# Optimization experiments

Hardware: AMD Instinct MI355X
Metric: run time of the kernel (lower is better)

## Reference

```python
import jax, jax.numpy as jnp
import numpy as np

HEADS = 16  # init kwarg 'heads'

def setup_inputs() -> dict:
    key = jax.random.key(0)
    k1, k2, k3 = jax.random.split(key, 3)
    B, S, D = 2, 2048, 1024
    x = jax.random.normal(k1, (B, S, D), dtype=jnp.float32)
    # nn.Linear(dim, 3*dim, bias=False): y = x @ W^T; store as [D, 3D] already transposed.
    w_qkv = jax.random.normal(k2, (D, 3 * D), dtype=jnp.float32) * 0.02
    w_out = jax.random.normal(k3, (D, D), dtype=jnp.float32) * 0.02
    return {"x": x, "w_qkv": w_qkv, "w_out": w_out}

def reference(x, w_qkv, w_out):
    B, S, D = x.shape
    H = HEADS
    hd = D // H
    scale = 1.0 / jnp.sqrt(jnp.asarray(hd, dtype=x.dtype))
    qkv = x @ w_qkv                      # [B, S, 3D]
    q, k, v = jnp.split(qkv, 3, axis=-1)
    def to_heads(t):
        return t.reshape(B, S, H, hd).transpose(0, 2, 1, 3)  # [B, H, S, hd]
    q, k, v = to_heads(q), to_heads(k), to_heads(v)
    scores = jnp.einsum('bhqd,bhkd->bhqk', q, k) * scale      # [B, H, S, S]
    # causal mask: query i attends to keys j <= i
    causal = jnp.tril(jnp.ones((S, S), dtype=bool))
    scores = jnp.where(causal, scores, -jnp.inf)
    p = jax.nn.softmax(scores, axis=-1)  # online-softmax in the original == exact softmax
    o = jnp.einsum('bhqk,bhkd->bhqd', p, v)                   # [B, H, S, hd]
    out = o.transpose(0, 2, 1, 3).reshape(B, S, D)
    return out @ w_out
```

## Files before the change

kernel.cpp:

```cpp
#include <hip/hip_runtime.h>


typedef unsigned short u16;
typedef unsigned int   u32;
typedef __attribute__((ext_vector_type(4))) u16    u16x4;
typedef __attribute__((ext_vector_type(8))) u16    u16x8;
typedef __attribute__((ext_vector_type(4))) short  s16x4;
typedef __attribute__((ext_vector_type(8))) __bf16 bf16x8;
typedef __attribute__((ext_vector_type(4))) float  f32x4;
typedef __attribute__((ext_vector_type(16))) float f32x16;

#define DEV static __device__ __forceinline__

DEV u16 f2b(float f) {
  unsigned u = __float_as_uint(f);
  u += 0x7fffu + ((u >> 16) & 1u);
  return (u16)(u >> 16);
}

DEV void gload_lds16(const void* g, void* l) {
  __builtin_amdgcn_global_load_lds((const __attribute__((address_space(1))) void*)g,
                                   (__attribute__((address_space(3))) void*)l, 16, 0, 0);
}

DEV unsigned lds_off(const void* p) {
  return (unsigned)(unsigned long long)(const __attribute__((address_space(3))) void*)p;
}

DEV s16x4 tr_read(unsigned off) {
  s16x4 d;
  asm volatile("ds_read_b64_tr_b16 %0, %1" : "=v"(d) : "v"(off));
  return d;
}

DEV u32 cvt_pk(float lo, float hi) {
  u32 r;
  asm("v_cvt_pk_bf16_f32 %0, %1, %2" : "=v"(r) : "v"(lo), "v"(hi));
  return r;
}

DEV void pswap(u32& x, u32& y) {
  asm volatile("v_permlane32_swap_b32 %0, %1" : "+v"(x), "+v"(y));
}

DEV f32x4 mfma32(bf16x8 a, bf16x8 b, f32x4 c) {
  return __builtin_amdgcn_mfma_f32_16x16x32_bf16(a, b, c, 0, 0, 0);
}
DEV f32x16 mfma3232(bf16x8 a, bf16x8 b, f32x16 c) {
  return __builtin_amdgcn_mfma_f32_32x32x16_bf16(a, b, c, 0, 0, 0);
}

__global__ __launch_bounds__(256) void cvt_kernel(const float* __restrict__ in,
                                                  u16* __restrict__ out, int n4) {
  int i = blockIdx.x * 256 + threadIdx.x;
  if (i >= n4) return;
  const float4 v = ((const float4*)in)[i];
  u16x4 o = { f2b(v.x), f2b(v.y), f2b(v.z), f2b(v.w) };
  ((u16x4*)out)[i] = o;
}

__global__ __launch_bounds__(256) void transpose_cvt(const float* __restrict__ w,
                                                     u16* __restrict__ wt,
                                                     const int Kdim, const int Ndim,
                                                     const int scaleN) {
  __shared__ u16 ls[32][33];
  const int tn = blockIdx.x * 32, tk = blockIdx.y * 32;
  const int t = threadIdx.x;
  const int r = t >> 3, c4 = (t & 7) * 4;
  const float s = (tn < scaleN) ? 0.18033688011112042f : 1.0f;
  float4 v = *(const float4*)(w + (size_t)(tk + r) * Ndim + tn + c4);
  ls[r][c4 + 0] = f2b(v.x * s); ls[r][c4 + 1] = f2b(v.y * s);
  ls[r][c4 + 2] = f2b(v.z * s); ls[r][c4 + 3] = f2b(v.w * s);
  __syncthreads();
  u16x4 ov = { ls[c4 + 0][r], ls[c4 + 1][r], ls[c4 + 2][r], ls[c4 + 3][r] };
  *(u16x4*)(wt + (size_t)(tn + r) * Kdim + tk + c4) = ov;
}

template<bool OUT_BF16>
__global__ __launch_bounds__(256) void gemm_bt(const u16* __restrict__ A,
                                               const u16* __restrict__ Bt,
                                               void* __restrict__ C, const int ldc) {
  const int tm = blockIdx.y * 128;
  const int tn = blockIdx.x * 128;
  const int tid = threadIdx.x;
  const int wave = tid >> 6, lane = tid & 63;
  const int wr = wave >> 1, wc = wave & 1;
  const int lg = lane >> 4, lc = lane & 15;
  __shared__ __align__(128) u16 lsA[128 * 32];
  __shared__ __align__(128) u16 lsB[128 * 32];

  f32x4 acc[4][4];
#pragma unroll
  for (int i = 0; i < 4; ++i)
#pragma unroll
    for (int j = 0; j < 4; ++j) acc[i][j] = (f32x4){0.f, 0.f, 0.f, 0.f};

  for (int kt = 0; kt < 32; ++kt) {
#pragma unroll
    for (int c = 0; c < 2; ++c) {
      const int p = tid + c * 256;
      const int row = p >> 2, ck = p & 3;
      const int cg = ck ^ ((row >> 1) & 3);
      gload_lds16(A  + (size_t)(tm + row) * 1024 + kt * 32 + cg * 8, (char*)lsA + p * 16);
      gload_lds16(Bt + (size_t)(tn + row) * 1024 + kt * 32 + cg * 8, (char*)lsB + p * 16);
    }
    __syncthreads();
    bf16x8 af[4], bg[4];
#pragma unroll
    for (int i = 0; i < 4; ++i) {
      const int ar = wr * 64 + i * 16 + lc;
      af[i] = *(const bf16x8*)(lsA + ar * 32 + (lg ^ ((ar >> 1) & 3)) * 8);
      const int br = wc * 64 + i * 16 + lc;
      bg[i] = *(const bf16x8*)(lsB + br * 32 + (lg ^ ((br >> 1) & 3)) * 8);
    }
#pragma unroll
    for (int i = 0; i < 4; ++i)
#pragma unroll
      for (int j = 0; j < 4; ++j)
        acc[i][j] = mfma32(af[i], bg[j], acc[i][j]);
    __syncthreads();
  }

#pragma unroll
  for (int i = 0; i < 4; ++i) {
#pragma unroll
    for (int r = 0; r < 4; ++r) {
      const int m = tm + wr * 64 + i * 16 + lg * 4 + r;
#pragma unroll
      for (int j = 0; j < 4; ++j) {
        const int n = tn + wc * 64 + j * 16 + lc;
        if (OUT_BF16) ((u16*)C)[(size_t)m * ldc + n] = f2b(acc[i][j][r]);
        else          ((float*)C)[(size_t)m * ldc + n] = acc[i][j][r];
      }
    }
  }
}

__global__ __launch_bounds__(128, 2) void attn_kernel(const u16* __restrict__ qkv,
                                                      u16* __restrict__ o) {
  const int p   = blockIdx.x >> 5;
  const int bh  = blockIdx.x & 31;
  const int b   = bh >> 4, h = bh & 15;
  const int tid  = threadIdx.x;
  const int wave = tid >> 6, lane = tid & 63;
  const int l31 = lane & 31, lg2 = lane >> 5;

  __shared__ __align__(128) char smem[2][16384];
  char* wb = smem[wave];

  const size_t bS = (size_t)b * 2048;

  unsigned koff[4], voff[4];
#pragma unroll
  for (int c = 0; c < 4; ++c) {
    const int pp_ = c * 64 + lane;
    {
      const int row = pp_ >> 3;
      const int cg = (pp_ & 7) ^ (row & 7);
      koff[c] = (unsigned)(row * 3072 + 1024 + h * 64 + cg * 8);
    }
    {
      const int s = pp_ >> 3, cw = pp_ & 7;
      voff[c] = (unsigned)((4 * (s >> 2) + (cw >> 1)) * 3072 + 2048 + h * 64
                           + (s & 3) * 16 + (cw & 1) * 8);
    }
  }

  auto STAGE = [&](int t, int bf) {
    const u16* base = qkv + (bS + (size_t)t * 32) * 3072;
    char* kd = wb + bf * 8192;
#pragma unroll
    for (int c = 0; c < 4; ++c)
      gload_lds16(base + koff[c], kd + (c * 64 + lane) * 16);
#pragma unroll
    for (int c = 0; c < 4; ++c)
      gload_lds16(base + voff[c], kd + 4096 + (c * 64 + lane) * 16);
  };

  auto run_qtile = [&](int qb) {
    const int T  = qb + 1;
    const int q0 = qb * 32;

    const u16* qrow = qkv + (bS + q0 + l31) * 3072 + h * 64;
    bf16x8 qf[4];
#pragma unroll
    for (int m = 0; m < 4; ++m)
      qf[m] = *(const bf16x8*)(qrow + 16 * m + 8 * lg2);

    float lsum = 0.f;
    f32x16 accO[2];
#pragma unroll
    for (int r = 0; r < 16; ++r) { accO[0][r] = 0.f; accO[1][r] = 0.f; }

    if (wave < T) STAGE(wave, 0);
    if (wave + 2 < T) STAGE(wave + 2, 1);

    int bf = 0;
    for (int t = wave; t < T; t += 2, bf ^= 1) {
      if (t + 2 < T) { asm volatile("s_waitcnt vmcnt(8)" ::: "memory"); }
      else           { asm volatile("s_waitcnt vmcnt(0)" ::: "memory"); }
      __builtin_amdgcn_sched_barrier(0);

      const u16* kbp = (const u16*)(wb + bf * 8192) + l31 * 64;
      bf16x8 kf[4];
#pragma unroll
      for (int m = 0; m < 4; ++m)
        kf[m] = *(const bf16x8*)(kbp + (((2 * m + lg2) ^ (l31 & 7)) * 8));
      f32x16 sc;
#pragma unroll
      for (int r = 0; r < 16; ++r) sc[r] = 0.f;
      __builtin_amdgcn_s_setprio(1);
#pragma unroll
      for (int m = 0; m < 4; ++m)
        sc = mfma3232(kf[m], qf[m], sc);
      __builtin_amdgcn_s_setprio(0);

      const unsigned vb = lds_off(wb + bf * 8192 + 4096);
      s16x4 vr[2][2][2];
#pragma unroll
      for (int db = 0; db < 2; ++db)
#pragma unroll
        for (int hh = 0; hh < 2; ++hh) {
          const unsigned a0 = vb +
            (unsigned)(((4 * hh + 2 * lg2) * 4 + db * 2 + (l31 >> 4)) * 128 + (l31 & 15) * 8);
          vr[db][hh][0] = tr_read(a0);
          vr[db][hh][1] = tr_read(a0 + 512);
        }

      float pp[16];
      if (t == T - 1) {
#pragma unroll
        for (int r = 0; r < 16; ++r) {
          const int kvp = (r & 3) + 8 * (r >> 2) + 4 * lg2;
          pp[r] = (kvp <= l31) ? exp2f(sc[r]) : 0.f;
        }
      } else {
#pragma unroll
        for (int r = 0; r < 16; ++r) pp[r] = exp2f(sc[r]);
      }
#pragma unroll
      for (int r = 0; r < 16; ++r) lsum += pp[r];

      asm volatile("s_waitcnt lgkmcnt(0)" ::: "memory");
      __builtin_amdgcn_sched_barrier(0);
      if (t + 4 < T) STAGE(t + 4, bf);
      __builtin_amdgcn_sched_barrier(0);

      u32 a01 = cvt_pk(pp[0], pp[1]),   a23 = cvt_pk(pp[2], pp[3]);
      u32 b01 = cvt_pk(pp[4], pp[5]),   b23 = cvt_pk(pp[6], pp[7]);
      u32 c01 = cvt_pk(pp[8], pp[9]),   c23 = cvt_pk(pp[10], pp[11]);
      u32 d01 = cvt_pk(pp[12], pp[13]), d23 = cvt_pk(pp[14], pp[15]);
      pswap(a01, b01); pswap(a23, b23);
      pswap(c01, d01); pswap(c23, d23);
      union Frag { u32 w[4]; bf16x8 v; };
      Frag f0, f1;
      f0.w[0] = a01; f0.w[1] = a23; f0.w[2] = b01; f0.w[3] = b23;
      f1.w[0] = c01; f1.w[1] = c23; f1.w[2] = d01; f1.w[3] = d23;

      __builtin_amdgcn_s_setprio(1);
#pragma unroll
      for (int db = 0; db < 2; ++db) {
        union { s16x4 hh[2]; bf16x8 v; } u0, u1;
        u0.hh[0] = vr[db][0][0]; u0.hh[1] = vr[db][0][1];
        u1.hh[0] = vr[db][1][0]; u1.hh[1] = vr[db][1][1];
        accO[db] = mfma3232(f0.v, u0.v, accO[db]);
        accO[db] = mfma3232(f1.v, u1.v, accO[db]);
      }
      __builtin_amdgcn_s_setprio(0);
    }

    lsum += __shfl_xor(lsum, 32);
    float* mO = (float*)wb;
    float* mL = (float*)(wb + 8192);
#pragma unroll
    for (int db = 0; db < 2; ++db)
#pragma unroll
      for (int r = 0; r < 16; ++r) {
        const int qp = (r & 3) + 8 * (r >> 2) + 4 * lg2;
        mO[qp * 64 + db * 32 + l31] = accO[db][r];
      }
    if (lane < 32) mL[l31] = lsum;
    __syncthreads();

    const float* O0 = (const float*)smem[0];
    const float* O1 = (const float*)smem[1];
    const float* L0 = (const float*)(smem[0] + 8192);
    const float* L1 = (const float*)(smem[1] + 8192);
    const int q  = wave * 16 + (lane >> 2);
    const int d0 = (lane & 3) * 16;
    const float inv = 1.f / (L0[q] + L1[q]);
    u16x8 ov[2];
#pragma unroll
    for (int j = 0; j < 4; ++j) {
      const f32x4 a = *(const f32x4*)(O0 + q * 64 + d0 + j * 4);
      const f32x4 c = *(const f32x4*)(O1 + q * 64 + d0 + j * 4);
#pragma unroll
      for (int e = 0; e < 4; ++e)
        ov[j >> 1][(j & 1) * 4 + e] = f2b((a[e] + c[e]) * inv);
    }
    const size_t orow = (bS + q0 + q) * 1024 + h * 64 + d0;
    *(u16x8*)(o + orow)     = ov[0];
    *(u16x8*)(o + orow + 8) = ov[1];
    __syncthreads();
  };

  run_qtile(p);
  run_qtile(63 - p);
}

extern "C" void kernel_launch(void* const* d_in, const int* in_sizes, int n_in,
                              void* d_out, int out_size, void* d_ws, size_t ws_size,
                              hipStream_t stream) {
  const float* x     = (const float*)d_in[0];
  const float* w_qkv = (const float*)d_in[1];
  const float* w_out = (const float*)d_in[2];
  float* out = (float*)d_out;
  char* ws = (char*)d_ws;

  u16* xb    = (u16*)(ws + 0);
  u16* wqkvT = (u16*)(ws + 8388608);
  u16* woutT = (u16*)(ws + 14680064);
  u16* qkvb  = (u16*)(ws + 16777216);
  u16* ob    = (u16*)(ws + 41943040);

  cvt_kernel<<<4096, 256, 0, stream>>>(x, xb, 1048576);
  transpose_cvt<<<dim3(96, 32), 256, 0, stream>>>(w_qkv, wqkvT, 1024, 3072, 1024);
  transpose_cvt<<<dim3(32, 32), 256, 0, stream>>>(w_out, woutT, 1024, 1024, 0);
  gemm_bt<true ><<<dim3(24, 32), 256, 0, stream>>>(xb, wqkvT, (void*)qkvb, 3072);
  attn_kernel<<<1024, 128, 0, stream>>>(qkvb, ob);
  gemm_bt<false><<<dim3(8, 32), 256, 0, stream>>>(ob, woutT, (void*)out, 1024);
}
```

Baseline: 118.8 us.

## Use one query tile per block, single-buffer K/V, double the grid

The attention kernel previously processed a pair of query tiles per block (p and 63-p) with double-buffered K/V staging in 32KB of LDS. Now each block handles one query tile, ordered largest-first, with a single 8KB-per-wave staging buffer and separate small LDS for row sums, and the grid doubles to 2048 blocks. The goal is to cut LDS per block so more blocks fit per CU and rely on hardware scheduling for causal load balance. In exchange, each wave now waits for its K/V tile with no prefetch overlap.

```diff
diff --git a/kernel.cpp b/kernel.cpp
--- a/kernel.cpp
+++ b/kernel.cpp
@@ -138,174 +138,161 @@
 
 __global__ __launch_bounds__(128, 2) void attn_kernel(const u16* __restrict__ qkv,
                                                       u16* __restrict__ o) {
-  const int p   = blockIdx.x >> 5;
+  const int qb  = 63 - (int)(blockIdx.x >> 5);
   const int bh  = blockIdx.x & 31;
   const int b   = bh >> 4, h = bh & 15;
   const int tid  = threadIdx.x;
   const int wave = tid >> 6, lane = tid & 63;
   const int l31 = lane & 31, lg2 = lane >> 5;
 
-  __shared__ __align__(128) char smem[2][16384];
+  __shared__ __align__(128) char smem[2][8192];
+  __shared__ float lsm[2][32];
   char* wb = smem[wave];
+  const unsigned vb = lds_off(wb + 4096);
 
   const size_t bS = (size_t)b * 2048;
+  const int T  = qb + 1;
+  const int q0 = qb * 32;
+
+  const u16* qrow = qkv + (bS + q0 + l31) * 3072 + h * 64;
+  bf16x8 qf[4];
+#pragma unroll
+  for (int m = 0; m < 4; ++m)
+    qf[m] = *(const bf16x8*)(qrow + 16 * m + 8 * lg2);
 
   unsigned koff[4], voff[4];
 #pragma unroll
   for (int c = 0; c < 4; ++c) {
-    const int pp_ = c * 64 + lane;
+    const int p = c * 64 + lane;
     {
-      const int row = pp_ >> 3;
-      const int cg = (pp_ & 7) ^ (row & 7);
+      const int row = p >> 3;
+      const int cg = (p & 7) ^ (row & 7);
       koff[c] = (unsigned)(row * 3072 + 1024 + h * 64 + cg * 8);
     }
     {
-      const int s = pp_ >> 3, cw = pp_ & 7;
+      const int s = p >> 3, cw = p & 7;
       voff[c] = (unsigned)((4 * (s >> 2) + (cw >> 1)) * 3072 + 2048 + h * 64
                            + (s & 3) * 16 + (cw & 1) * 8);
     }
   }
 
-  auto STAGE = [&](int t, int bf) {
+  auto STAGE = [&](int t) {
     const u16* base = qkv + (bS + (size_t)t * 32) * 3072;
-    char* kd = wb + bf * 8192;
 #pragma unroll
     for (int c = 0; c < 4; ++c)
-      gload_lds16(base + koff[c], kd + (c * 64 + lane) * 16);
+      gload_lds16(base + koff[c], wb + (c * 64 + lane) * 16);
 #pragma unroll
     for (int c = 0; c < 4; ++c)
-      gload_lds16(base + voff[c], kd + 4096 + (c * 64 + lane) * 16);
+      gload_lds16(base + voff[c], wb + 4096 + (c * 64 + lane) * 16);
   };
 
-  auto run_qtile = [&](int qb) {
-    const int T  = qb + 1;
-    const int q0 = qb * 32;
-
-    const u16* qrow = qkv + (bS + q0 + l31) * 3072 + h * 64;
-    bf16x8 qf[4];
+  float lsum = 0.f;
+  f32x16 accO[2];
+#pragma unroll
+  for (int r = 0; r < 16; ++r) { accO[0][r] = 0.f; accO[1][r] = 0.f; }
+
+  if (wave < T) STAGE(wave);
+
+  for (int t = wave; t < T; t += 2) {
+    asm volatile("s_waitcnt vmcnt(0)" ::: "memory");
+    __builtin_amdgcn_sched_barrier(0);
+
+    const u16* kbp = (const u16*)wb + l31 * 64;
+    bf16x8 kf[4];
 #pragma unroll
     for (int m = 0; m < 4; ++m)
-      qf[m] = *(const bf16x8*)(qrow + 16 * m + 8 * lg2);
-
-    float lsum = 0.f;
-    f32x16 accO[2];
-#pragma unroll
-    for (int r = 0; r < 16; ++r) { accO[0][r] = 0.f; accO[1][r] = 0.f; }
-
-    if (wave < T) STAGE(wave, 0);
-    if (wave + 2 < T) STAGE(wave + 2, 1);
-
-    int bf = 0;
-    for (int t = wave; t < T; t += 2, bf ^= 1) {
-      if (t + 2 < T) { asm volatile("s_waitcnt vmcnt(8)" ::: "memory"); }
-      else           { asm volatile("s_waitcnt vmcnt(0)" ::: "memory"); }
-      __builtin_amdgcn_sched_barrier(0);
-
-      const u16* kbp = (const u16*)(wb + bf * 8192) + l31 * 64;
-      bf16x8 kf[4];
-#pragma unroll
-      for (int m = 0; m < 4; ++m)
-        kf[m] = *(const bf16x8*)(kbp + (((2 * m + lg2) ^ (l31 & 7)) * 8));
-      f32x16 sc;
-#pragma unroll
-      for (int r = 0; r < 16; ++r) sc[r] = 0.f;
-      __builtin_amdgcn_s_setprio(1);
-#pragma unroll
-      for (int m = 0; m < 4; ++m)
-        sc = mfma3232(kf[m], qf[m], sc);
-      __builtin_amdgcn_s_setprio(0);
-
-      const unsigned vb = lds_off(wb + bf * 8192 + 4096);
-      s16x4 vr[2][2][2];
-#pragma unroll
-      for (int db = 0; db < 2; ++db)
-#pragma unroll
-        for (int hh = 0; hh < 2; ++hh) {
-          const unsigned a0 = vb +
-            (unsigned)(((4 * hh + 2 * lg2) * 4 + db * 2 + (l31 >> 4)) * 128 + (l31 & 15) * 8);
-          vr[db][hh][0] = tr_read(a0);
-          vr[db][hh][1] = tr_read(a0 + 512);
-        }
-
-      float pp[16];
-      if (t == T - 1) {
-#pragma unroll
-        for (int r = 0; r < 16; ++r) {
-          const int kvp = (r & 3) + 8 * (r >> 2) + 4 * lg2;
-          pp[r] = (kvp <= l31) ? exp2f(sc[r]) : 0.f;
-        }
-      } else {
-#pragma unroll
-        for (int r = 0; r < 16; ++r) pp[r] = exp2f(sc[r]);
+      kf[m] = *(const bf16x8*)(kbp + (((2 * m + lg2) ^ (l31 & 7)) * 8));
+    f32x16 sc;
+#pragma unroll
+    for (int r = 0; r < 16; ++r) sc[r] = 0.f;
+    __builtin_amdgcn_s_setprio(1);
+#pragma unroll
+    for (int m = 0; m < 4; ++m)
+      sc = mfma3232(kf[m], qf[m], sc);
+    __builtin_amdgcn_s_setprio(0);
+
+    s16x4 vr[2][2][2];
+#pragma unroll
+    for (int db = 0; db < 2; ++db)
+#pragma unroll
+      for (int hh = 0; hh < 2; ++hh) {
+        const unsigned a0 = vb +
+          (unsigned)(((4 * hh + 2 * lg2) * 4 + db * 2 + (l31 >> 4)) * 128 + (l31 & 15) * 8);
+        vr[db][hh][0] = tr_read(a0);
+        vr[db][hh][1] = tr_read(a0 + 512);
       }
-#pragma unroll
-      for (int r = 0; r < 16; ++r) lsum += pp[r];
-
-      asm volatile("s_waitcnt lgkmcnt(0)" ::: "memory");
-      __builtin_amdgcn_sched_barrier(0);
-      if (t + 4 < T) STAGE(t + 4, bf);
-      __builtin_amdgcn_sched_barrier(0);
-
-      u32 a01 = cvt_pk(pp[0], pp[1]),   a23 = cvt_pk(pp[2], pp[3]);
-      u32 b01 = cvt_pk(pp[4], pp[5]),   b23 = cvt_pk(pp[6], pp[7]);
-      u32 c01 = cvt_pk(pp[8], pp[9]),   c23 = cvt_pk(pp[10], pp[11]);
-      u32 d01 = cvt_pk(pp[12], pp[13]), d23 = cvt_pk(pp[14], pp[15]);
-      pswap(a01, b01); pswap(a23, b23);
-      pswap(c01, d01); pswap(c23, d23);
-      union Frag { u32 w[4]; bf16x8 v; };
-      Frag f0, f1;
-      f0.w[0] = a01; f0.w[1] = a23; f0.w[2] = b01; f0.w[3] = b23;
-      f1.w[0] = c01; f1.w[1] = c23; f1.w[2] = d01; f1.w[3] = d23;
-
-      __builtin_amdgcn_s_setprio(1);
-#pragma unroll
-      for (int db = 0; db < 2; ++db) {
-        union { s16x4 hh[2]; bf16x8 v; } u0, u1;
-        u0.hh[0] = vr[db][0][0]; u0.hh[1] = vr[db][0][1];
-        u1.hh[0] = vr[db][1][0]; u1.hh[1] = vr[db][1][1];
-        accO[db] = mfma3232(f0.v, u0.v, accO[db]);
-        accO[db] = mfma3232(f1.v, u1.v, accO[db]);
+
+    float pp[16];
+    if (t == T - 1) {
+#pragma unroll
+      for (int r = 0; r < 16; ++r) {
+        const int kvp = (r & 3) + 8 * (r >> 2) + 4 * lg2;
+        pp[r] = (kvp <= l31) ? exp2f(sc[r]) : 0.f;
       }
-      __builtin_amdgcn_s_setprio(0);
-    }
-
-    lsum += __shfl_xor(lsum, 32);
-    float* mO = (float*)wb;
-    float* mL = (float*)(wb + 8192);
-#pragma unroll
-    for (int db = 0; db < 2; ++db)
-#pragma unroll
-      for (int r = 0; r < 16; ++r) {
-        const int qp = (r & 3) + 8 * (r >> 2) + 4 * lg2;
-        mO[qp * 64 + db * 32 + l31] = accO[db][r];
-      }
-    if (lane < 32) mL[l31] = lsum;
-    __syncthreads();
-
-    const float* O0 = (const float*)smem[0];
-    const float* O1 = (const float*)smem[1];
-    const float* L0 = (const float*)(smem[0] + 8192);
-    const float* L1 = (const float*)(smem[1] + 8192);
-    const int q  = wave * 16 + (lane >> 2);
-    const int d0 = (lane & 3) * 16;
-    const float inv = 1.f / (L0[q] + L1[q]);
-    u16x8 ov[2];
-#pragma unroll
-    for (int j = 0; j < 4; ++j) {
-      const f32x4 a = *(const f32x4*)(O0 + q * 64 + d0 + j * 4);
-      const f32x4 c = *(const f32x4*)(O1 + q * 64 + d0 + j * 4);
-#pragma unroll
-      for (int e = 0; e < 4; ++e)
-        ov[j >> 1][(j & 1) * 4 + e] = f2b((a[e] + c[e]) * inv);
-    }
-    const size_t orow = (bS + q0 + q) * 1024 + h * 64 + d0;
-    *(u16x8*)(o + orow)     = ov[0];
-    *(u16x8*)(o + orow + 8) = ov[1];
-    __syncthreads();
-  };
-
-  run_qtile(p);
-  run_qtile(63 - p);
+    } else {
+#pragma unroll
+      for (int r = 0; r < 16; ++r) pp[r] = exp2f(sc[r]);
+    }
+#pragma unroll
+    for (int r = 0; r < 16; ++r) lsum += pp[r];
+
+    asm volatile("s_waitcnt lgkmcnt(0)" ::: "memory");
+    __builtin_amdgcn_sched_barrier(0);
+    if (t + 2 < T) STAGE(t + 2);
+    __builtin_amdgcn_sched_barrier(0);
+
+    u32 a01 = cvt_pk(pp[0], pp[1]),   a23 = cvt_pk(pp[2], pp[3]);
+    u32 b01 = cvt_pk(pp[4], pp[5]),   b23 = cvt_pk(pp[6], pp[7]);
+    u32 c01 = cvt_pk(pp[8], pp[9]),   c23 = cvt_pk(pp[10], pp[11]);
+    u32 d01 = cvt_pk(pp[12], pp[13]), d23 = cvt_pk(pp[14], pp[15]);
+    pswap(a01, b01); pswap(a23, b23);
+    pswap(c01, d01); pswap(c23, d23);
+    union Frag { u32 w[4]; bf16x8 v; };
+    Frag f0, f1;
+    f0.w[0] = a01; f0.w[1] = a23; f0.w[2] = b01; f0.w[3] = b23;
+    f1.w[0] = c01; f1.w[1] = c23; f1.w[2] = d01; f1.w[3] = d23;
+
+    __builtin_amdgcn_s_setprio(1);
+#pragma unroll
+    for (int db = 0; db < 2; ++db) {
+      union { s16x4 hh[2]; bf16x8 v; } u0, u1;
+      u0.hh[0] = vr[db][0][0]; u0.hh[1] = vr[db][0][1];
+      u1.hh[0] = vr[db][1][0]; u1.hh[1] = vr[db][1][1];
+      accO[db] = mfma3232(f0.v, u0.v, accO[db]);
+      accO[db] = mfma3232(f1.v, u1.v, accO[db]);
+    }
+    __builtin_amdgcn_s_setprio(0);
+  }
+
+  lsum += __shfl_xor(lsum, 32);
+  float* mO = (float*)wb;
+#pragma unroll
+  for (int db = 0; db < 2; ++db)
+#pragma unroll
+    for (int r = 0; r < 16; ++r) {
+      const int qp = (r & 3) + 8 * (r >> 2) + 4 * lg2;
+      mO[qp * 64 + db * 32 + l31] = accO[db][r];
+    }
+  if (lane < 32) lsm[wave][l31] = lsum;
+  __syncthreads();
+
+  const float* O0 = (const float*)smem[0];
+  const float* O1 = (const float*)smem[1];
+  const int q  = wave * 16 + (lane >> 2);
+  const int d0 = (lane & 3) * 16;
+  const float inv = 1.f / (lsm[0][q] + lsm[1][q]);
+  u16x8 ov[2];
+#pragma unroll
+  for (int j = 0; j < 4; ++j) {
+    const f32x4 a = *(const f32x4*)(O0 + q * 64 + d0 + j * 4);
+    const f32x4 c = *(const f32x4*)(O1 + q * 64 + d0 + j * 4);
+#pragma unroll
+    for (int e = 0; e < 4; ++e)
+      ov[j >> 1][(j & 1) * 4 + e] = f2b((a[e] + c[e]) * inv);
+  }
+  const size_t orow = (bS + q0 + q) * 1024 + h * 64 + d0;
+  *(u16x8*)(o + orow)     = ov[0];
+  *(u16x8*)(o + orow + 8) = ov[1];
 }
 
 extern "C" void kernel_launch(void* const* d_in, const int* in_sizes, int n_in,
@@ -327,6 +314,6 @@
   transpose_cvt<<<dim3(96, 32), 256, 0, stream>>>(w_qkv, wqkvT, 1024, 3072, 1024);
   transpose_cvt<<<dim3(32, 32), 256, 0, stream>>>(w_out, woutT, 1024, 1024, 0);
   gemm_bt<true ><<<dim3(24, 32), 256, 0, stream>>>(xb, wqkvT, (void*)qkvb, 3072);
-  attn_kernel<<<1024, 128, 0, stream>>>(qkvb, ob);
+  attn_kernel<<<2048, 128, 0, stream>>>(qkvb, ob);
   gemm_bt<false><<<dim3(8, 32), 256, 0, stream>>>(ob, woutT, (void*)out, 1024);
 }
```

Result: faster. 110.8 us (-6.7%).
